# Kernel optimization log

Hardware: AMD Instinct MI355X
Metric: run time of the kernel (lower is better)

The kernel has to match this reference:

```python
import jax, jax.numpy as jnp
import numpy as np

N_NODES = 100000
N_EDGES = 1600000
D_IN = 64
D_OUT = 64


def setup_inputs() -> dict:
    key = jax.random.key(0)
    k1, k2, k3, k4, k5 = jax.random.split(key, 5)
    x = jax.random.normal(k1, (N_NODES, D_IN), dtype=jnp.float32)
    edge_src = jax.random.randint(k2, (N_EDGES,), 0, N_NODES, dtype=jnp.int32)
    edge_dst = jax.random.randint(k3, (N_EDGES,), 0, N_NODES, dtype=jnp.int32)
    edge_val = jnp.ones((N_EDGES,), dtype=jnp.float32)
    stdv = 1.0 / np.sqrt(D_OUT)
    weight = jax.random.uniform(k4, (D_IN, D_OUT), minval=-stdv, maxval=stdv, dtype=jnp.float32)
    epsilon = jnp.ones((1,), dtype=jnp.float32)
    bias = jax.random.uniform(k5, (D_OUT,), minval=-stdv, maxval=stdv, dtype=jnp.float32)
    return {"x": x, "edge_src": edge_src, "edge_dst": edge_dst,
            "edge_val": edge_val, "weight": weight, "epsilon": epsilon, "bias": bias}


def reference(x, edge_src, edge_dst, edge_val, weight, epsilon, bias):
    # spmm(adj, x): row i of adj gathers neighbors -> segment_sum over edge_src
    # adj[i, j] = edge_val for edge (src=i, dst=j)
    msgs = edge_val[:, None] * x[edge_dst]            # [E, D_in]
    agg = jax.ops.segment_sum(msgs, edge_src, num_segments=N_NODES)  # [N, D_in]
    # epsilon * eye(N) @ x == epsilon * x (avoid O(N^2) identity)
    rep = agg + epsilon * x                            # [N, D_in]
    out = rep @ weight + bias                          # [N, D_out]
    return out, rep
```

## Files before the change

### kernel.cpp

```cpp
#include <hip/hip_runtime.h>
#include <hip/hip_fp16.h>

#define N_NODES 100000
#define N_EDGES 1600000
#define D 64

#define NB 391
#define BLKA 391
#define EPB 4096
#define NT (NB * BLKA)
#define NCH 150

#define WS_GHIST   0
#define WS_PART    152896
#define WS_ROWPTR  153152
#define WS_PAIRSU  253184
#define WS_XH      1853184

__global__ __launch_bounds__(256) void k_hist_cvt(
    const int* __restrict__ esrc, const float* __restrict__ x,
    int* __restrict__ ghist, uint2* __restrict__ xh2)
{
    __shared__ int h[NB];
    int t = threadIdx.x;
    for (int j = t; j < NB; j += 256) h[j] = 0;
    __syncthreads();
    int base = blockIdx.x * EPB;
    #pragma unroll
    for (int i = 0; i < 4; ++i) {
        int e0 = base + i * 1024 + t * 4;
        if (e0 < N_EDGES) {
            int4 s4 = *(const int4*)(esrc + e0);
            atomicAdd(&h[s4.x >> 8], 1);
            atomicAdd(&h[s4.y >> 8], 1);
            atomicAdd(&h[s4.z >> 8], 1);
            atomicAdd(&h[s4.w >> 8], 1);
        }
    }
    {
        const float4* x4 = (const float4*)x;
        #pragma unroll
        for (int i = 0; i < 16; ++i) {
            int f = blockIdx.x * 4096 + i * 256 + t;
            if (f < N_NODES * (D / 4)) {
                float4 v = x4[f];
                uint2 o;
                o.x = (uint)__half_as_ushort(__float2half_rn(v.x)) |
                      ((uint)__half_as_ushort(__float2half_rn(v.y)) << 16);
                o.y = (uint)__half_as_ushort(__float2half_rn(v.z)) |
                      ((uint)__half_as_ushort(__float2half_rn(v.w)) << 16);
                xh2[f] = o;
            }
        }
    }
    __syncthreads();
    for (int j = t; j < NB; j += 256) ghist[j * BLKA + blockIdx.x] = h[j];
}

__global__ __launch_bounds__(1024) void k_scan1(
    const int* __restrict__ ghist, int* __restrict__ partial)
{
    __shared__ int sred[16];
    int t = threadIdx.x;
    int idx = blockIdx.x * 1024 + t;
    int v = (idx < NT) ? ghist[idx] : 0;
    #pragma unroll
    for (int off = 32; off; off >>= 1) v += __shfl_down(v, off, 64);
    if ((t & 63) == 0) sred[t >> 6] = v;
    __syncthreads();
    if (t < 16) {
        int w = sred[t];
        #pragma unroll
        for (int off = 8; off; off >>= 1) w += __shfl_down(w, off, 16);
        if (t == 0) partial[blockIdx.x] = w;
    }
}

__global__ __launch_bounds__(1024) void k_scan2(
    int* __restrict__ ghist, const int* __restrict__ partial)
{
    __shared__ int red1[16];
    __shared__ int wsum[16];
    __shared__ int bc;
    int t = threadIdx.x;
    int lane = t & 63, wid = t >> 6;

    int pv = (t < NCH) ? partial[t] : 0;
    int a1 = (t < (int)blockIdx.x) ? pv : 0;
    #pragma unroll
    for (int off = 32; off; off >>= 1) a1 += __shfl_down(a1, off, 64);
    if (lane == 0) red1[wid] = a1;
    __syncthreads();
    if (t < 16) {
        int w = red1[t];
        #pragma unroll
        for (int off = 8; off; off >>= 1) w += __shfl_down(w, off, 16);
        if (t == 0) bc = w;
    }
    __syncthreads();

    int idx = blockIdx.x * 1024 + t;
    int v = (idx < NT) ? ghist[idx] : 0;
    int s = v;
    #pragma unroll
    for (int off = 1; off < 64; off <<= 1) {
        int y = __shfl_up(s, off, 64);
        if (lane >= off) s += y;
    }
    if (lane == 63) wsum[wid] = s;
    __syncthreads();
    if (t < 16) {
        int w = wsum[t];
        #pragma unroll
        for (int off = 1; off < 16; off <<= 1) {
            int y = __shfl_up(w, off, 16);
            if (t >= off) w += y;
        }
        wsum[t] = w;
    }
    __syncthreads();
    int prefix = wid ? wsum[wid - 1] : 0;
    if (idx < NT) ghist[idx] = bc + prefix + s - v;
}

__global__ __launch_bounds__(256) void k_scatter(
    const int* __restrict__ esrc, const int* __restrict__ edst,
    const float* __restrict__ eval_, const int* __restrict__ ghist,
    int2* __restrict__ tpairs)
{
    __shared__ int base[NB];
    int t = threadIdx.x;
    for (int j = t; j < NB; j += 256) base[j] = ghist[j * BLKA + blockIdx.x];
    __syncthreads();
    int eb = blockIdx.x * EPB;
    #pragma unroll
    for (int i = 0; i < 4; ++i) {
        int e0 = eb + i * 1024 + t * 4;
        if (e0 < N_EDGES) {
            int4 s4 = *(const int4*)(esrc + e0);
            int4 d4 = *(const int4*)(edst + e0);
            float4 v4 = *(const float4*)(eval_ + e0);
            int p0 = atomicAdd(&base[s4.x >> 8], 1);
            int p1 = atomicAdd(&base[s4.y >> 8], 1);
            int p2 = atomicAdd(&base[s4.z >> 8], 1);
            int p3 = atomicAdd(&base[s4.w >> 8], 1);
            tpairs[p0] = make_int2(((s4.x & 255) << 17) | d4.x, __float_as_int(v4.x));
            tpairs[p1] = make_int2(((s4.y & 255) << 17) | d4.y, __float_as_int(v4.y));
            tpairs[p2] = make_int2(((s4.z & 255) << 17) | d4.z, __float_as_int(v4.z));
            tpairs[p3] = make_int2(((s4.w & 255) << 17) | d4.w, __float_as_int(v4.w));
        }
    }
}

__global__ __launch_bounds__(256) void k_build(
    const int2* __restrict__ tpairs, const int* __restrict__ ghist,
    int* __restrict__ row_ptr, unsigned int* __restrict__ pairsu)
{
    __shared__ int hist[256], cursor[256], wsum4[4];
    int b = blockIdx.x, t = threadIdx.x;
    int s_begin = ghist[b * BLKA];
    int s_end = (b + 1 < NB) ? ghist[(b + 1) * BLKA] : N_EDGES;
    hist[t] = 0;
    __syncthreads();
    #pragma unroll 4
    for (int pos = s_begin + t; pos < s_end; pos += 256)
        atomicAdd(&hist[(tpairs[pos].x >> 17) & 255], 1);
    __syncthreads();
    int lane = t & 63, wid = t >> 6;
    int v = hist[t], s = v;
    #pragma unroll
    for (int off = 1; off < 64; off <<= 1) {
        int y = __shfl_up(s, off, 64);
        if (lane >= off) s += y;
    }
    if (lane == 63) wsum4[wid] = s;
    __syncthreads();
    if (t == 0) {
        int r = 0;
        #pragma unroll
        for (int k = 0; k < 4; ++k) { int w = wsum4[k]; wsum4[k] = r; r += w; }
    }
    __syncthreads();
    int excl = wsum4[wid] + s - v;
    cursor[t] = excl;
    int node = (b << 8) + t;
    if (node <= N_NODES) row_ptr[node] = s_begin + excl;
    __syncthreads();
    #pragma unroll 4
    for (int pos = s_begin + t; pos < s_end; pos += 256) {
        int2 pv = tpairs[pos];
        int k = (pv.x >> 17) & 255;
        int p = atomicAdd(&cursor[k], 1);
        unsigned int dst = (unsigned int)pv.x & 0x1FFFFu;
        unsigned int hb = (unsigned int)__half_as_ushort(
            __float2half_rn(__int_as_float(pv.y)));
        pairsu[s_begin + p] = (dst << 15) | (hb >> 1);
    }
}

#define GATHER_BLOCKS 2048

__global__ __launch_bounds__(256) void k_gather(
    const float* __restrict__ x, const uint2* __restrict__ xh2,
    const int* __restrict__ row_ptr, const unsigned int* __restrict__ pairsu,
    const float* __restrict__ epsilon, float* __restrict__ rep)
{
    int w = (blockIdx.x * 256 + threadIdx.x) >> 6;
    int nw = gridDim.x * 4;
    int lane = threadIdx.x & 63;
    int sub = lane >> 4;
    int f4 = lane & 15;
    float eps = epsilon[0];
    const float4* x4 = (const float4*)x;

    int r0 = (int)((long long)w * N_NODES / nw);
    int r1 = (int)((long long)(w + 1) * N_NODES / nw);

    for (int row = r0; row < r1; ++row) {
        int start = __builtin_amdgcn_readfirstlane(row_ptr[row]);
        int end   = __builtin_amdgcn_readfirstlane(row_ptr[row + 1]);
        float4 acc = make_float4(0.f, 0.f, 0.f, 0.f);
        for (int j = start; j < end; j += 16) {
            unsigned int pk[4];
            #pragma unroll
            for (int u = 0; u < 4; ++u) {
                int e = j + u * 4 + sub;
                pk[u] = (e < end) ? pairsu[e] : 0u;
            }
            uint2 a[4];
            #pragma unroll
            for (int u = 0; u < 4; ++u)
                a[u] = xh2[(size_t)(pk[u] >> 15) * 16 + f4];
            #pragma unroll
            for (int u = 0; u < 4; ++u) {
                unsigned short hb = (unsigned short)((pk[u] & 0x7FFFu) << 1);
                float vv = __half2float(__ushort_as_half(hb));
                float2 f01 = __half22float2(*reinterpret_cast<const __half2*>(&a[u].x));
                float2 f23 = __half22float2(*reinterpret_cast<const __half2*>(&a[u].y));
                acc.x += vv * f01.x; acc.y += vv * f01.y;
                acc.z += vv * f23.x; acc.w += vv * f23.y;
            }
        }
        #pragma unroll
        for (int off = 16; off <= 32; off <<= 1) {
            acc.x += __shfl_xor(acc.x, off, 64);
            acc.y += __shfl_xor(acc.y, off, 64);
            acc.z += __shfl_xor(acc.z, off, 64);
            acc.w += __shfl_xor(acc.w, off, 64);
        }
        if (sub == 0) {
            float4 xv = x4[(size_t)row * 16 + f4];
            float4 o = make_float4(acc.x + eps * xv.x, acc.y + eps * xv.y,
                                   acc.z + eps * xv.z, acc.w + eps * xv.w);
            ((float4*)rep)[(size_t)row * 16 + f4] = o;
        }
    }
}

#define GEMM_TM 64
__global__ __launch_bounds__(256) void k_gemm(
    const float* __restrict__ rep, const float* __restrict__ weight,
    const float* __restrict__ bias, float* __restrict__ out)
{
    __shared__ float rep_s[GEMM_TM * 68];
    __shared__ float Ws[D * D];
    int t = threadIdx.x;
    {
        const float4* w4 = (const float4*)weight;
        float4* s4 = (float4*)Ws;
        #pragma unroll
        for (int i = 0; i < (D * D / 4) / 256; ++i)
            s4[t + i * 256] = w4[t + i * 256];
    }
    int row0 = blockIdx.x * GEMM_TM;
    {
        const float4* r4 = (const float4*)rep;
        #pragma unroll
        for (int i = 0; i < 4; ++i) {
            int f = t + i * 256;
            int rr = f >> 4, kk4 = f & 15;
            float4 v = (row0 + rr < N_NODES) ? r4[(size_t)(row0 + rr) * 16 + kk4]
                                             : make_float4(0.f, 0.f, 0.f, 0.f);
            rep_s[rr * 68 + kk4 * 4 + 0] = v.x;
            rep_s[rr * 68 + kk4 * 4 + 1] = v.y;
            rep_s[rr * 68 + kk4 * 4 + 2] = v.z;
            rep_s[rr * 68 + kk4 * 4 + 3] = v.w;
        }
    }
    __syncthreads();

    int tx = t & 15, ty = t >> 4;
    float4 b4 = ((const float4*)bias)[tx];
    float acc[4][4];
    #pragma unroll
    for (int i = 0; i < 4; ++i) {
        acc[i][0] = b4.x; acc[i][1] = b4.y; acc[i][2] = b4.z; acc[i][3] = b4.w;
    }
    #pragma unroll 4
    for (int k4 = 0; k4 < 16; ++k4) {
        float4 rv[4];
        #pragma unroll
        for (int i = 0; i < 4; ++i)
            rv[i] = *(const float4*)&rep_s[(ty * 4 + i) * 68 + k4 * 4];
        #pragma unroll
        for (int kk = 0; kk < 4; ++kk) {
            float4 wv = *(const float4*)&Ws[(k4 * 4 + kk) * D + tx * 4];
            #pragma unroll
            for (int i = 0; i < 4; ++i) {
                float r = ((const float*)&rv[i])[kk];
                acc[i][0] += r * wv.x;
                acc[i][1] += r * wv.y;
                acc[i][2] += r * wv.z;
                acc[i][3] += r * wv.w;
            }
        }
    }
    #pragma unroll
    for (int i = 0; i < 4; ++i) {
        int row = row0 + ty * 4 + i;
        if (row < N_NODES)
            *(float4*)&out[(size_t)row * D + tx * 4] =
                make_float4(acc[i][0], acc[i][1], acc[i][2], acc[i][3]);
    }
}

extern "C" void kernel_launch(void* const* d_in, const int* in_sizes, int n_in,
                              void* d_out, int out_size, void* d_ws, size_t ws_size,
                              hipStream_t stream) {
    const float* x    = (const float*)d_in[0];
    const int*   esrc = (const int*)  d_in[1];
    const int*   edst = (const int*)  d_in[2];
    const float* ev   = (const float*)d_in[3];
    const float* w    = (const float*)d_in[4];
    const float* eps  = (const float*)d_in[5];
    const float* bias = (const float*)d_in[6];

    float* out = (float*)d_out;
    float* rep = out + (size_t)N_NODES * D;

    int* ws       = (int*)d_ws;
    int* ghist    = ws + WS_GHIST;
    int* partial  = ws + WS_PART;
    int* row_ptr  = ws + WS_ROWPTR;
    unsigned int* pairsu = (unsigned int*)(ws + WS_PAIRSU);
    uint2* xh2    = (uint2*)(ws + WS_XH);
    int2* tpairs  = (int2*)rep;

    k_hist_cvt<<<BLKA, 256, 0, stream>>>(esrc, x, ghist, xh2);
    k_scan1<<<NCH, 1024, 0, stream>>>(ghist, partial);
    k_scan2<<<NCH, 1024, 0, stream>>>(ghist, partial);
    k_scatter<<<BLKA, 256, 0, stream>>>(esrc, edst, ev, ghist, tpairs);
    k_build<<<NB, 256, 0, stream>>>(tpairs, ghist, row_ptr, pairsu);
    k_gather<<<GATHER_BLOCKS, 256, 0, stream>>>(x, xh2, row_ptr, pairsu, eps, rep);
    k_gemm<<<(N_NODES + GEMM_TM - 1) / GEMM_TM, 256, 0, stream>>>(rep, w, bias, out);
}
```

Before: 199.9 us.

## Fold scan into scatter, widen gather loads, use fp16 x for epsilon term

Removes the two scan kernels. Each scatter block now recomputes its bucket bases by summing a transposed histogram column, and block 0 writes the global bucket offsets used by the build kernel. The gather kernel loads 16-byte fp16 rows, so 8 lanes cover a row and 8 edges are processed per wave step, with two accumulators and an extra shuffle stage. It also reads the epsilon*x term from the fp16 copy instead of fp32 x, which lowers precision of rep. Each scatter block also redoes a 391-long strided loop over the histogram.

New measurement: 201.4 us. About the same (+0.8%).

```diff
diff --git a/kernel.cpp b/kernel.cpp
--- a/kernel.cpp
+++ b/kernel.cpp
@@ -8,27 +8,26 @@
 #define NB 391
 #define BLKA 391
 #define EPB 4096
-#define NT (NB * BLKA)
-#define NCH 150
+#define GST 400
 
 #define WS_GHIST   0
-#define WS_PART    152896
-#define WS_ROWPTR  153152
-#define WS_PAIRSU  253184
-#define WS_XH      1853184
-
-__global__ __launch_bounds__(256) void k_hist_cvt(
+#define WS_G       156416
+#define WS_ROWPTR  156832
+#define WS_PAIRSU  256864
+#define WS_XH      1856864
+
+__global__ __launch_bounds__(512) void k_hist_cvt(
     const int* __restrict__ esrc, const float* __restrict__ x,
     int* __restrict__ ghist, uint2* __restrict__ xh2)
 {
     __shared__ int h[NB];
-    int t = threadIdx.x;
-    for (int j = t; j < NB; j += 256) h[j] = 0;
-    __syncthreads();
-    int base = blockIdx.x * EPB;
-    #pragma unroll
-    for (int i = 0; i < 4; ++i) {
-        int e0 = base + i * 1024 + t * 4;
+    int t = threadIdx.x, blk = blockIdx.x;
+    if (t < NB) h[t] = 0;
+    __syncthreads();
+    int base = blk * EPB;
+    #pragma unroll
+    for (int i = 0; i < 2; ++i) {
+        int e0 = base + i * 2048 + t * 4;
         if (e0 < N_EDGES) {
             int4 s4 = *(const int4*)(esrc + e0);
             atomicAdd(&h[s4.x >> 8], 1);
@@ -40,68 +39,42 @@
     {
         const float4* x4 = (const float4*)x;
         #pragma unroll
-        for (int i = 0; i < 16; ++i) {
-            int f = blockIdx.x * 4096 + i * 256 + t;
+        for (int i = 0; i < 8; ++i) {
+            int f = blk * 4096 + i * 512 + t;
             if (f < N_NODES * (D / 4)) {
                 float4 v = x4[f];
                 uint2 o;
-                o.x = (uint)__half_as_ushort(__float2half_rn(v.x)) |
-                      ((uint)__half_as_ushort(__float2half_rn(v.y)) << 16);
-                o.y = (uint)__half_as_ushort(__float2half_rn(v.z)) |
-                      ((uint)__half_as_ushort(__float2half_rn(v.w)) << 16);
+                o.x = (unsigned int)__half_as_ushort(__float2half_rn(v.x)) |
+                      ((unsigned int)__half_as_ushort(__float2half_rn(v.y)) << 16);
+                o.y = (unsigned int)__half_as_ushort(__float2half_rn(v.z)) |
+                      ((unsigned int)__half_as_ushort(__float2half_rn(v.w)) << 16);
                 xh2[f] = o;
             }
         }
     }
     __syncthreads();
-    for (int j = t; j < NB; j += 256) ghist[j * BLKA + blockIdx.x] = h[j];
-}
-
-__global__ __launch_bounds__(1024) void k_scan1(
-    const int* __restrict__ ghist, int* __restrict__ partial)
-{
-    __shared__ int sred[16];
-    int t = threadIdx.x;
-    int idx = blockIdx.x * 1024 + t;
-    int v = (idx < NT) ? ghist[idx] : 0;
-    #pragma unroll
-    for (int off = 32; off; off >>= 1) v += __shfl_down(v, off, 64);
-    if ((t & 63) == 0) sred[t >> 6] = v;
-    __syncthreads();
-    if (t < 16) {
-        int w = sred[t];
-        #pragma unroll
-        for (int off = 8; off; off >>= 1) w += __shfl_down(w, off, 16);
-        if (t == 0) partial[blockIdx.x] = w;
-    }
-}
-
-__global__ __launch_bounds__(1024) void k_scan2(
-    int* __restrict__ ghist, const int* __restrict__ partial)
-{
-    __shared__ int red1[16];
-    __shared__ int wsum[16];
-    __shared__ int bc;
-    int t = threadIdx.x;
+    if (t < NB) ghist[blk * GST + t] = h[t];
+}
+
+__global__ __launch_bounds__(512) void k_scatter(
+    const int* __restrict__ esrc, const int* __restrict__ edst,
+    const float* __restrict__ eval_, const int* __restrict__ ghist,
+    int* __restrict__ G, int2* __restrict__ tpairs)
+{
+    __shared__ int base[NB];
+    __shared__ int wsum[8];
+    int t = threadIdx.x, blk = blockIdx.x;
     int lane = t & 63, wid = t >> 6;
 
-    int pv = (t < NCH) ? partial[t] : 0;
-    int a1 = (t < (int)blockIdx.x) ? pv : 0;
-    #pragma unroll
-    for (int off = 32; off; off >>= 1) a1 += __shfl_down(a1, off, 64);
-    if (lane == 0) red1[wid] = a1;
-    __syncthreads();
-    if (t < 16) {
-        int w = red1[t];
-        #pragma unroll
-        for (int off = 8; off; off >>= 1) w += __shfl_down(w, off, 16);
-        if (t == 0) bc = w;
-    }
-    __syncthreads();
-
-    int idx = blockIdx.x * 1024 + t;
-    int v = (idx < NT) ? ghist[idx] : 0;
-    int s = v;
+    int tot = 0, P = 0;
+    if (t < NB) {
+        for (int c = 0; c < BLKA; ++c) {
+            int v = ghist[c * GST + t];
+            tot += v;
+            if (c < blk) P += v;
+        }
+    }
+    int s = tot;
     #pragma unroll
     for (int off = 1; off < 64; off <<= 1) {
         int y = __shfl_up(s, off, 64);
@@ -109,33 +82,26 @@
     }
     if (lane == 63) wsum[wid] = s;
     __syncthreads();
-    if (t < 16) {
-        int w = wsum[t];
-        #pragma unroll
-        for (int off = 1; off < 16; off <<= 1) {
-            int y = __shfl_up(w, off, 16);
-            if (t >= off) w += y;
-        }
-        wsum[t] = w;
-    }
-    __syncthreads();
-    int prefix = wid ? wsum[wid - 1] : 0;
-    if (idx < NT) ghist[idx] = bc + prefix + s - v;
-}
-
-__global__ __launch_bounds__(256) void k_scatter(
-    const int* __restrict__ esrc, const int* __restrict__ edst,
-    const float* __restrict__ eval_, const int* __restrict__ ghist,
-    int2* __restrict__ tpairs)
-{
-    __shared__ int base[NB];
-    int t = threadIdx.x;
-    for (int j = t; j < NB; j += 256) base[j] = ghist[j * BLKA + blockIdx.x];
-    __syncthreads();
-    int eb = blockIdx.x * EPB;
-    #pragma unroll
-    for (int i = 0; i < 4; ++i) {
-        int e0 = eb + i * 1024 + t * 4;
+    if (t == 0) {
+        int r = 0;
+        #pragma unroll
+        for (int k = 0; k < 8; ++k) { int v = wsum[k]; wsum[k] = r; r += v; }
+    }
+    __syncthreads();
+    int Gv = wsum[wid] + s - tot;
+    if (t < NB) {
+        base[t] = Gv + P;
+        if (blk == 0) {
+            G[t] = Gv;
+            if (t == NB - 1) G[NB] = Gv + tot;
+        }
+    }
+    __syncthreads();
+
+    int eb = blk * EPB;
+    #pragma unroll
+    for (int i = 0; i < 2; ++i) {
+        int e0 = eb + i * 2048 + t * 4;
         if (e0 < N_EDGES) {
             int4 s4 = *(const int4*)(esrc + e0);
             int4 d4 = *(const int4*)(edst + e0);
@@ -153,13 +119,13 @@
 }
 
 __global__ __launch_bounds__(256) void k_build(
-    const int2* __restrict__ tpairs, const int* __restrict__ ghist,
+    const int2* __restrict__ tpairs, const int* __restrict__ G,
     int* __restrict__ row_ptr, unsigned int* __restrict__ pairsu)
 {
     __shared__ int hist[256], cursor[256], wsum4[4];
     int b = blockIdx.x, t = threadIdx.x;
-    int s_begin = ghist[b * BLKA];
-    int s_end = (b + 1 < NB) ? ghist[(b + 1) * BLKA] : N_EDGES;
+    int s_begin = G[b];
+    int s_end   = G[b + 1];
     hist[t] = 0;
     __syncthreads();
     #pragma unroll 4
@@ -201,17 +167,16 @@
 #define GATHER_BLOCKS 2048
 
 __global__ __launch_bounds__(256) void k_gather(
-    const float* __restrict__ x, const uint2* __restrict__ xh2,
-    const int* __restrict__ row_ptr, const unsigned int* __restrict__ pairsu,
-    const float* __restrict__ epsilon, float* __restrict__ rep)
+    const uint4* __restrict__ xh4, const int* __restrict__ row_ptr,
+    const unsigned int* __restrict__ pairsu, const float* __restrict__ epsilon,
+    float* __restrict__ rep)
 {
     int w = (blockIdx.x * 256 + threadIdx.x) >> 6;
     int nw = gridDim.x * 4;
     int lane = threadIdx.x & 63;
-    int sub = lane >> 4;
-    int f4 = lane & 15;
+    int sub = lane >> 3;
+    int h8 = lane & 7;
     float eps = epsilon[0];
-    const float4* x4 = (const float4*)x;
 
     int r0 = (int)((long long)w * N_NODES / nw);
     int r1 = (int)((long long)(w + 1) * N_NODES / nw);
@@ -219,40 +184,56 @@
     for (int row = r0; row < r1; ++row) {
         int start = __builtin_amdgcn_readfirstlane(row_ptr[row]);
         int end   = __builtin_amdgcn_readfirstlane(row_ptr[row + 1]);
-        float4 acc = make_float4(0.f, 0.f, 0.f, 0.f);
-        for (int j = start; j < end; j += 16) {
-            unsigned int pk[4];
+        float4 accA = make_float4(0.f, 0.f, 0.f, 0.f);
+        float4 accB = make_float4(0.f, 0.f, 0.f, 0.f);
+        for (int j = start; j < end; j += 32) {
+            unsigned int pk[4]; uint4 a[4];
             #pragma unroll
             for (int u = 0; u < 4; ++u) {
-                int e = j + u * 4 + sub;
+                int e = j + u * 8 + sub;
                 pk[u] = (e < end) ? pairsu[e] : 0u;
             }
-            uint2 a[4];
             #pragma unroll
             for (int u = 0; u < 4; ++u)
-                a[u] = xh2[(size_t)(pk[u] >> 15) * 16 + f4];
+                a[u] = xh4[(size_t)(pk[u] >> 15) * 8 + h8];
             #pragma unroll
             for (int u = 0; u < 4; ++u) {
                 unsigned short hb = (unsigned short)((pk[u] & 0x7FFFu) << 1);
                 float vv = __half2float(__ushort_as_half(hb));
-                float2 f01 = __half22float2(*reinterpret_cast<const __half2*>(&a[u].x));
-                float2 f23 = __half22float2(*reinterpret_cast<const __half2*>(&a[u].y));
-                acc.x += vv * f01.x; acc.y += vv * f01.y;
-                acc.z += vv * f23.x; acc.w += vv * f23.y;
+                float2 f0 = __half22float2(*reinterpret_cast<const __half2*>(&a[u].x));
+                float2 f1 = __half22float2(*reinterpret_cast<const __half2*>(&a[u].y));
+                float2 f2 = __half22float2(*reinterpret_cast<const __half2*>(&a[u].z));
+                float2 f3 = __half22float2(*reinterpret_cast<const __half2*>(&a[u].w));
+                accA.x += vv * f0.x; accA.y += vv * f0.y;
+                accA.z += vv * f1.x; accA.w += vv * f1.y;
+                accB.x += vv * f2.x; accB.y += vv * f2.y;
+                accB.z += vv * f3.x; accB.w += vv * f3.y;
             }
         }
         #pragma unroll
-        for (int off = 16; off <= 32; off <<= 1) {
-            acc.x += __shfl_xor(acc.x, off, 64);
-            acc.y += __shfl_xor(acc.y, off, 64);
-            acc.z += __shfl_xor(acc.z, off, 64);
-            acc.w += __shfl_xor(acc.w, off, 64);
-        }
-        if (sub == 0) {
-            float4 xv = x4[(size_t)row * 16 + f4];
-            float4 o = make_float4(acc.x + eps * xv.x, acc.y + eps * xv.y,
-                                   acc.z + eps * xv.z, acc.w + eps * xv.w);
-            ((float4*)rep)[(size_t)row * 16 + f4] = o;
+        for (int off = 8; off <= 32; off <<= 1) {
+            accA.x += __shfl_xor(accA.x, off, 64);
+            accA.y += __shfl_xor(accA.y, off, 64);
+            accA.z += __shfl_xor(accA.z, off, 64);
+            accA.w += __shfl_xor(accA.w, off, 64);
+            accB.x += __shfl_xor(accB.x, off, 64);
+            accB.y += __shfl_xor(accB.y, off, 64);
+            accB.z += __shfl_xor(accB.z, off, 64);
+            accB.w += __shfl_xor(accB.w, off, 64);
+        }
+        if (lane < 8) {
+            uint4 xr = xh4[(size_t)row * 8 + lane];
+            float2 x0 = __half22float2(*reinterpret_cast<const __half2*>(&xr.x));
+            float2 x1 = __half22float2(*reinterpret_cast<const __half2*>(&xr.y));
+            float2 x2 = __half22float2(*reinterpret_cast<const __half2*>(&xr.z));
+            float2 x3 = __half22float2(*reinterpret_cast<const __half2*>(&xr.w));
+            float4* r4 = (float4*)rep;
+            r4[(size_t)row * 16 + lane * 2] =
+                make_float4(accA.x + eps * x0.x, accA.y + eps * x0.y,
+                            accA.z + eps * x1.x, accA.w + eps * x1.y);
+            r4[(size_t)row * 16 + lane * 2 + 1] =
+                make_float4(accB.x + eps * x2.x, accB.y + eps * x2.y,
+                            accB.z + eps * x3.x, accB.w + eps * x3.y);
         }
     }
 }
@@ -340,17 +321,16 @@
 
     int* ws       = (int*)d_ws;
     int* ghist    = ws + WS_GHIST;
-    int* partial  = ws + WS_PART;
+    int* G        = ws + WS_G;
     int* row_ptr  = ws + WS_ROWPTR;
     unsigned int* pairsu = (unsigned int*)(ws + WS_PAIRSU);
     uint2* xh2    = (uint2*)(ws + WS_XH);
+    uint4* xh4    = (uint4*)(ws + WS_XH);
     int2* tpairs  = (int2*)rep;
 
-    k_hist_cvt<<<BLKA, 256, 0, stream>>>(esrc, x, ghist, xh2);
-    k_scan1<<<NCH, 1024, 0, stream>>>(ghist, partial);
-    k_scan2<<<NCH, 1024, 0, stream>>>(ghist, partial);
-    k_scatter<<<BLKA, 256, 0, stream>>>(esrc, edst, ev, ghist, tpairs);
-    k_build<<<NB, 256, 0, stream>>>(tpairs, ghist, row_ptr, pairsu);
-    k_gather<<<GATHER_BLOCKS, 256, 0, stream>>>(x, xh2, row_ptr, pairsu, eps, rep);
+    k_hist_cvt<<<BLKA, 512, 0, stream>>>(esrc, x, ghist, xh2);
+    k_scatter<<<BLKA, 512, 0, stream>>>(esrc, edst, ev, ghist, G, tpairs);
+    k_build<<<NB, 256, 0, stream>>>(tpairs, G, row_ptr, pairsu);
+    k_gather<<<GATHER_BLOCKS, 256, 0, stream>>>(xh4, row_ptr, pairsu, eps, rep);
     k_gemm<<<(N_NODES + GEMM_TM - 1) / GEMM_TM, 256, 0, stream>>>(rep, w, bias, out);
 }
```
